# Kernel optimization log

Measured on AMD Instinct MI355X. Metric: run time of the kernel, lower is better.

Reference implementation:

```python
import jax, jax.numpy as jnp
from jax import lax
import numpy as np

B = 1024
CH = 32          # decomp.channel
LEVEL = 3        # decomp.level
CTOT = CH * (LEVEL + 1)   # 128, ODE state dim == GRU input dim
T_POINTS = 96    # decomp.eval_time_points
PRED_LEN = 96
HID = 128


def _dopri5_traj(y0, ts, Wo, bo):
    """Fixed-grid Dormand-Prince 5(4) integration of dy/dt = tanh(y Wo^T + bo).
    y0: [B, CTOT]; ts: [T]. Returns trajectory [T, B, CTOT]."""
    f = lambda y: jnp.tanh(y @ Wo.T + bo)

    def step(y, dt):
        k1 = f(y)
        k2 = f(y + dt * (0.2 * k1))
        k3 = f(y + dt * (3.0 / 40 * k1 + 9.0 / 40 * k2))
        k4 = f(y + dt * (44.0 / 45 * k1 - 56.0 / 15 * k2 + 32.0 / 9 * k3))
        k5 = f(y + dt * (19372.0 / 6561 * k1 - 25360.0 / 2187 * k2 + 64448.0 / 6561 * k3 - 212.0 / 729 * k4))
        k6 = f(y + dt * (9017.0 / 3168 * k1 - 355.0 / 33 * k2 + 46732.0 / 5247 * k3 + 49.0 / 176 * k4 - 5103.0 / 18656 * k5))
        y_next = y + dt * (35.0 / 384 * k1 + 500.0 / 1113 * k3 + 125.0 / 192 * k4 - 2187.0 / 6784 * k5 + 11.0 / 84 * k6)
        return y_next, y_next

    _, ys = lax.scan(step, y0, ts[1:] - ts[:-1])
    return jnp.concatenate([y0[None], ys], axis=0)


def _gru_layer(xs, W_ih, W_hh, b_ih, b_hh):
    """PyTorch-semantics GRU layer. xs: [T, B, D] -> hidden states [T, B, H]."""
    gi = jnp.einsum('tbd,gd->tbg', xs, W_ih) + b_ih  # precompute input gates
    H = W_hh.shape[1]

    def cell(h, gi_t):
        gh = h @ W_hh.T + b_hh
        i_r, i_z, i_n = jnp.split(gi_t, 3, axis=-1)
        h_r, h_z, h_n = jnp.split(gh, 3, axis=-1)
        r = jax.nn.sigmoid(i_r + h_r)
        z = jax.nn.sigmoid(i_z + h_z)
        n = jnp.tanh(i_n + r * h_n)
        h_new = (1.0 - z) * n + z * h
        return h_new, h_new

    h0 = jnp.zeros((xs.shape[1], H), xs.dtype)
    _, hs = lax.scan(cell, h0, gi)
    return hs


def setup_inputs() -> dict:
    key = jax.random.key(0)
    ks = jax.random.split(key, 20)
    s = 0.08  # ~1/sqrt(128), keeps GRU/ODE in a stable regime
    return {
        'x': jax.random.normal(ks[0], (B, CH, 256), jnp.float32),
        'yl': jax.random.normal(ks[1], (B, CH, 1), jnp.float32),
        'yh': jax.random.normal(ks[2], (B, CH * LEVEL, 1), jnp.float32),
        'W_ode': jax.random.normal(ks[3], (CTOT, CTOT), jnp.float32) * 0.05,
        'b_ode': jax.random.normal(ks[4], (CTOT,), jnp.float32) * 0.05,
        'W_ih0': jax.random.normal(ks[5], (3 * HID, CTOT), jnp.float32) * s,
        'W_hh0': jax.random.normal(ks[6], (3 * HID, HID), jnp.float32) * s,
        'b_ih0': jax.random.normal(ks[7], (3 * HID,), jnp.float32) * s,
        'b_hh0': jax.random.normal(ks[8], (3 * HID,), jnp.float32) * s,
        'W_ih1': jax.random.normal(ks[9], (3 * HID, HID), jnp.float32) * s,
        'W_hh1': jax.random.normal(ks[10], (3 * HID, HID), jnp.float32) * s,
        'b_ih1': jax.random.normal(ks[11], (3 * HID,), jnp.float32) * s,
        'b_hh1': jax.random.normal(ks[12], (3 * HID,), jnp.float32) * s,
        'W1': jax.random.normal(ks[13], (64, HID), jnp.float32) * s,
        'b1': jax.random.normal(ks[14], (64,), jnp.float32) * s,
        'W2': jax.random.normal(ks[15], (PRED_LEN * CH, 64), jnp.float32) * 0.125,
        'b2': jax.random.normal(ks[16], (PRED_LEN * CH,), jnp.float32) * 0.125,
    }


def reference(x, yl, yh, W_ode, b_ode,
              W_ih0, W_hh0, b_ih0, b_hh0,
              W_ih1, W_hh1, b_ih1, b_hh1,
              W1, b1, W2, b2):
    # coeffs = cat([yl] + yh, dim=1) -> [B, CTOT, 1] -> squeeze coeff length (=1)
    coeffs = jnp.concatenate([yl, yh], axis=1)[..., 0]  # [B, CTOT]
    ts = jnp.linspace(0.0, 1.0, T_POINTS)
    traj = _dopri5_traj(coeffs, ts, W_ode, b_ode)  # [T, B, CTOT]
    # rearrange 't b c l -> b t (c l)' with l == 1; GRU scans over leading T axis
    h1 = _gru_layer(traj, W_ih0, W_hh0, b_ih0, b_hh0)   # [T, B, HID]
    h2 = _gru_layer(h1, W_ih1, W_hh1, b_ih1, b_hh1)     # [T, B, HID]
    last = h2[-1]                                        # [B, HID]
    hidden = jax.nn.gelu(last @ W1.T + b1, approximate=False)
    pred = hidden @ W2.T + b2                            # [B, PRED_LEN*CH]
    return pred.reshape(-1, CH, PRED_LEN)
```

## Files before the change

kernel.cpp:

```cpp
#include <hip/hip_runtime.h>
#include <hip/hip_bf16.h>
#include <math.h>

#define TPTS 96
#define CTOT 128
#define LDP 134

typedef __bf16 bf16x8_t __attribute__((ext_vector_type(8)));
typedef float f32x4_t __attribute__((ext_vector_type(4)));
typedef unsigned short us8_t __attribute__((ext_vector_type(8)));

__device__ __forceinline__ unsigned short f2b(float f) {
    union { float f; unsigned int i; } v; v.f = f;
    unsigned int r = v.i + 0x7fffu + ((v.i >> 16) & 1u);
    return (unsigned short)(r >> 16);
}
__device__ __forceinline__ unsigned int packbf2(float a, float b) {
    return (unsigned int)f2b(a) | ((unsigned int)f2b(b) << 16);
}
__device__ __forceinline__ uint2 pack4(float v0, float v1, float v2, float v3) {
    uint2 w; w.x = packbf2(v0, v1); w.y = packbf2(v2, v3); return w;
}
__device__ __forceinline__ f32x4_t mfma16(bf16x8_t a, bf16x8_t b, f32x4_t c) {
    return __builtin_amdgcn_mfma_f32_16x16x32_bf16(a, b, c, 0, 0, 0);
}
__device__ __forceinline__ bf16x8_t ldfrag(const unsigned short* p) {
    us8_t v = *(const us8_t*)p;
    return __builtin_bit_cast(bf16x8_t, v);
}
__device__ __forceinline__ bf16x8_t ldfragG(const unsigned short* p) {
    union { unsigned long long q[2]; us8_t v; } u;
    u.q[0] = __hip_atomic_load((const unsigned long long*)p,
                               __ATOMIC_RELAXED, __HIP_MEMORY_SCOPE_AGENT);
    u.q[1] = __hip_atomic_load((const unsigned long long*)(p + 4),
                               __ATOMIC_RELAXED, __HIP_MEMORY_SCOPE_AGENT);
    return __builtin_bit_cast(bf16x8_t, u.v);
}
__device__ __forceinline__ void stg8(unsigned short* p, uint2 pk) {
    unsigned long long q = ((unsigned long long)pk.y << 32) | (unsigned long long)pk.x;
    __hip_atomic_store((unsigned long long*)p, q,
                       __ATOMIC_RELAXED, __HIP_MEMORY_SCOPE_AGENT);
}
__device__ __forceinline__ bf16x8_t ldfragW(const float* p) {
    float4 a = *(const float4*)p;
    float4 b = *(const float4*)(p + 4);
    bf16x8_t r;
    r[0] = __builtin_bit_cast(__bf16, f2b(a.x)); r[1] = __builtin_bit_cast(__bf16, f2b(a.y));
    r[2] = __builtin_bit_cast(__bf16, f2b(a.z)); r[3] = __builtin_bit_cast(__bf16, f2b(a.w));
    r[4] = __builtin_bit_cast(__bf16, f2b(b.x)); r[5] = __builtin_bit_cast(__bf16, f2b(b.y));
    r[6] = __builtin_bit_cast(__bf16, f2b(b.z)); r[7] = __builtin_bit_cast(__bf16, f2b(b.w));
    return r;
}
__device__ __forceinline__ float tanh2(float x) {
    float e = __expf(x + x);
    return 1.f - __fdividef(2.f, e + 1.f);
}
__device__ __forceinline__ float sigm(float x) {
    return __fdividef(1.f, 1.f + __expf(-x));
}

__device__ __forceinline__ void waitflag(unsigned int* f, unsigned int want) {
    if (threadIdx.x == 0) {
        int guard = 0;
        while (__hip_atomic_load(f, __ATOMIC_RELAXED, __HIP_MEMORY_SCOPE_AGENT) != want) {
            __builtin_amdgcn_s_sleep(2);
            if (++guard > (1 << 21)) break;
        }
    }
    __syncthreads();
}
__device__ __forceinline__ void setflag(unsigned int* f, unsigned int val) {
    if (threadIdx.x == 0) {
        asm volatile("s_waitcnt vmcnt(0)" ::: "memory");
        __hip_atomic_store(f, val, __ATOMIC_RELAXED, __HIP_MEMORY_SCOPE_AGENT);
    }
}

__global__ void __launch_bounds__(512, 2)
ode_forecaster(const float* __restrict__ yl,
               const float* __restrict__ yh,
               const float* __restrict__ Wode,
               const float* __restrict__ bode,
               const float* __restrict__ Wih0,
               const float* __restrict__ Whh0,
               const float* __restrict__ bih0,
               const float* __restrict__ bhh0,
               const float* __restrict__ Wih1,
               const float* __restrict__ Whh1,
               const float* __restrict__ bih1,
               const float* __restrict__ bhh1,
               const float* __restrict__ W1v,
               const float* __restrict__ b1v,
               const float* __restrict__ W2v,
               const float* __restrict__ b2v,
               float* __restrict__ outp,
               char* __restrict__ wsb)
{
    const int role = blockIdx.x >> 6;
    const int c    = blockIdx.x & 63;
    const int tid  = threadIdx.x, lane = tid & 63, wv = tid >> 6;
    const int l15  = lane & 15, quad = lane >> 4;
    const int fbase = wv * 16 + quad * 4;
    const int rbase = c * 16;

    __shared__ __align__(16) unsigned short zbuf[2][16][LDP];
    __shared__ __align__(16) unsigned short hidbuf[16][72];

    unsigned short* yTraj  = (unsigned short*)(wsb);
    unsigned short* h1Traj = (unsigned short*)(wsb + 0x2000000);
    unsigned int*   yflag  = (unsigned int*)(wsb + 0x4000000);
    unsigned int*   h1flag = (unsigned int*)(wsb + 0x4010000);
#define YMAGIC(t)  (0x5E000000u + (unsigned)(t))
#define H1MAGIC(t) (0x6E000000u + (unsigned)(t))

    if (role == 0) {
        bf16x8_t wode[4];
#pragma unroll
        for (int kt = 0; kt < 4; ++kt)
            wode[kt] = ldfragW(Wode + (wv * 16 + l15) * CTOT + kt * 32 + quad * 8);
        float bo[4];
        {
            float4 b4 = *(const float4*)(bode + fbase);
            bo[0] = b4.x; bo[1] = b4.y; bo[2] = b4.z; bo[3] = b4.w;
        }
        float y[4];
        {
            int row = rbase + l15;
#pragma unroll
            for (int i = 0; i < 4; ++i) {
                int f = fbase + i;
                y[i] = (f < 32) ? yl[row * 32 + f] : yh[row * 96 + (f - 32)];
            }
            uint2 pk = pack4(y[0], y[1], y[2], y[3]);
            *(uint2*)&zbuf[0][l15][fbase] = pk;
            stg8(yTraj + ((size_t)row) * CTOT + fbase, pk);
        }
        __syncthreads();
        setflag(&yflag[c * 128 + 0], YMAGIC(0));

        const float dt = 1.0f / 95.0f;
        const float d10 = dt * 0.2f;
        const float d20 = dt * (3.f/40.f),  d21 = dt * (9.f/40.f);
        const float d30 = dt * (44.f/45.f), d31 = dt * (-56.f/15.f), d32 = dt * (32.f/9.f);
        const float d40 = dt * (19372.f/6561.f), d41 = dt * (-25360.f/2187.f),
                    d42 = dt * (64448.f/6561.f), d43 = dt * (-212.f/729.f);
        const float d50 = dt * (9017.f/3168.f), d51 = dt * (-355.f/33.f),
                    d52 = dt * (46732.f/5247.f), d53 = dt * (49.f/176.f),
                    d54 = dt * (-5103.f/18656.f);
        const float e0 = dt * (35.f/384.f), e2 = dt * (500.f/1113.f), e3 = dt * (125.f/192.f),
                    e4 = dt * (-2187.f/6784.f), e5 = dt * (11.f/84.f);

        int p = 0;
        float kr[6][4];
#pragma unroll 1
        for (int t = 0; t < 95; ++t) {
#pragma unroll
            for (int s = 0; s < 6; ++s) {
                bf16x8_t bf[4];
#pragma unroll
                for (int kt = 0; kt < 4; ++kt)
                    bf[kt] = ldfrag(&zbuf[p][l15][kt * 32 + quad * 8]);
                f32x4_t a0 = {0.f, 0.f, 0.f, 0.f}, a1 = {0.f, 0.f, 0.f, 0.f};
                a0 = mfma16(wode[0], bf[0], a0);
                a1 = mfma16(wode[1], bf[1], a1);
                a0 = mfma16(wode[2], bf[2], a0);
                a1 = mfma16(wode[3], bf[3], a1);
                f32x4_t acc = a0 + a1;
#pragma unroll
                for (int i = 0; i < 4; ++i) kr[s][i] = tanh2(acc[i] + bo[i]);

                if (s < 5) {
                    float z[4];
#pragma unroll
                    for (int i = 0; i < 4; ++i) {
                        float zv;
                        if (s == 0)      zv = y[i] + d10 * kr[0][i];
                        else if (s == 1) zv = y[i] + d20 * kr[0][i] + d21 * kr[1][i];
                        else if (s == 2) zv = y[i] + d30 * kr[0][i] + d31 * kr[1][i] + d32 * kr[2][i];
                        else if (s == 3) zv = y[i] + d40 * kr[0][i] + d41 * kr[1][i]
                                             + d42 * kr[2][i] + d43 * kr[3][i];
                        else             zv = y[i] + d50 * kr[0][i] + d51 * kr[1][i]
                                             + d52 * kr[2][i] + d53 * kr[3][i] + d54 * kr[4][i];
                        z[i] = zv;
                    }
                    *(uint2*)&zbuf[p ^ 1][l15][fbase] = pack4(z[0], z[1], z[2], z[3]);
                } else {
#pragma unroll
                    for (int i = 0; i < 4; ++i)
                        y[i] += e0*kr[0][i] + e2*kr[2][i] + e3*kr[3][i] + e4*kr[4][i] + e5*kr[5][i];
                    uint2 pk = pack4(y[0], y[1], y[2], y[3]);
                    *(uint2*)&zbuf[p ^ 1][l15][fbase] = pk;
                    stg8(yTraj + ((size_t)(t + 1) * 1024 + rbase + l15) * CTOT + fbase, pk);
                }
                __syncthreads();
                p ^= 1;
                if (s == 5) setflag(&yflag[c * 128 + t + 1], YMAGIC(t + 1));
            }
        }
        return;
    }

    const float* Wih = (role == 1) ? Wih0 : Wih1;
    const float* Whh = (role == 1) ? Whh0 : Whh1;
    const float* bih = (role == 1) ? bih0 : bih1;
    const float* bhh = (role == 1) ? bhh0 : bhh1;
    const unsigned short* src = (role == 1) ? yTraj : h1Traj;
    unsigned int* sflag = (role == 1) ? yflag : h1flag;

    bf16x8_t wih[3][4], whh[3][4];
#pragma unroll
    for (int g = 0; g < 3; ++g)
#pragma unroll
        for (int kt = 0; kt < 4; ++kt) {
            wih[g][kt] = ldfragW(Wih + (size_t)(g * 128 + wv * 16 + l15) * CTOT + kt * 32 + quad * 8);
            whh[g][kt] = ldfragW(Whh + (size_t)(g * 128 + wv * 16 + l15) * CTOT + kt * 32 + quad * 8);
        }
    float br[4], bz[4], bin_[4], bhn[4];
    {
        float4 a0 = *(const float4*)(bih + 0 * 128 + fbase);
        float4 b0 = *(const float4*)(bhh + 0 * 128 + fbase);
        float4 a1 = *(const float4*)(bih + 1 * 128 + fbase);
        float4 b1 = *(const float4*)(bhh + 1 * 128 + fbase);
        float4 a2 = *(const float4*)(bih + 2 * 128 + fbase);
        float4 b2 = *(const float4*)(bhh + 2 * 128 + fbase);
        br[0] = a0.x + b0.x; br[1] = a0.y + b0.y; br[2] = a0.z + b0.z; br[3] = a0.w + b0.w;
        bz[0] = a1.x + b1.x; bz[1] = a1.y + b1.y; bz[2] = a1.z + b1.z; bz[3] = a1.w + b1.w;
        bin_[0] = a2.x; bin_[1] = a2.y; bin_[2] = a2.z; bin_[3] = a2.w;
        bhn[0] = b2.x; bhn[1] = b2.y; bhn[2] = b2.z; bhn[3] = b2.w;
    }

    float h[4] = {0.f, 0.f, 0.f, 0.f};
    *(uint2*)&zbuf[0][l15][fbase] = pack4(0.f, 0.f, 0.f, 0.f);
    int p = 0;
    __syncthreads();

#pragma unroll 1
    for (int t = 0; t < TPTS; ++t) {
        waitflag(&sflag[c * 128 + t], (role == 1) ? YMAGIC(t) : H1MAGIC(t));
        const unsigned short* xp = src + ((size_t)t * 1024 + rbase + l15) * CTOT;
        bf16x8_t ax[4], ah[4];
#pragma unroll
        for (int kt = 0; kt < 4; ++kt) {
            ax[kt] = ldfragG(xp + kt * 32 + quad * 8);
            ah[kt] = ldfrag(&zbuf[p][l15][kt * 32 + quad * 8]);
        }
        f32x4_t gx[3], gh[3];
#pragma unroll
        for (int g = 0; g < 3; ++g) {
            gx[g] = (f32x4_t){0.f, 0.f, 0.f, 0.f};
            gh[g] = (f32x4_t){0.f, 0.f, 0.f, 0.f};
        }
#pragma unroll
        for (int kt = 0; kt < 4; ++kt) {
            gx[0] = mfma16(wih[0][kt], ax[kt], gx[0]);
            gx[1] = mfma16(wih[1][kt], ax[kt], gx[1]);
            gx[2] = mfma16(wih[2][kt], ax[kt], gx[2]);
            gh[0] = mfma16(whh[0][kt], ah[kt], gh[0]);
            gh[1] = mfma16(whh[1][kt], ah[kt], gh[1]);
            gh[2] = mfma16(whh[2][kt], ah[kt], gh[2]);
        }
#pragma unroll
        for (int i = 0; i < 4; ++i) {
            float rr = sigm(gx[0][i] + gh[0][i] + br[i]);
            float zz = sigm(gx[1][i] + gh[1][i] + bz[i]);
            float nn = tanh2((gx[2][i] + bin_[i]) + rr * (gh[2][i] + bhn[i]));
            h[i] = nn + zz * (h[i] - nn);
        }
        uint2 pk = pack4(h[0], h[1], h[2], h[3]);
        *(uint2*)&zbuf[p ^ 1][l15][fbase] = pk;
        if (role == 1)
            stg8(h1Traj + ((size_t)t * 1024 + rbase + l15) * CTOT + fbase, pk);
        __syncthreads();
        if (role == 1) setflag(&h1flag[c * 128 + t], H1MAGIC(t));
        p ^= 1;
    }
    if (role == 1) return;

    if (wv < 4) {
        bf16x8_t wf[4], hf[4];
#pragma unroll
        for (int kt = 0; kt < 4; ++kt) {
            wf[kt] = ldfragW(W1v + (size_t)(wv * 16 + l15) * CTOT + kt * 32 + quad * 8);
            hf[kt] = ldfrag(&zbuf[p][l15][kt * 32 + quad * 8]);
        }
        f32x4_t acc = {0.f, 0.f, 0.f, 0.f};
#pragma unroll
        for (int kt = 0; kt < 4; ++kt) acc = mfma16(wf[kt], hf[kt], acc);
        float4 bb = *(const float4*)(b1v + wv * 16 + quad * 4);
        const float* bbp = (const float*)&bb;
        float gl[4];
#pragma unroll
        for (int i = 0; i < 4; ++i) {
            float x = acc[i] + bbp[i];
            gl[i] = 0.5f * x * (1.0f + erff(x * 0.70710678118654752f));
        }
        *(uint2*)&hidbuf[l15][wv * 16 + quad * 4] = pack4(gl[0], gl[1], gl[2], gl[3]);
    }
    __syncthreads();

    bf16x8_t ahid[2];
#pragma unroll
    for (int kt = 0; kt < 2; ++kt)
        ahid[kt] = ldfrag(&hidbuf[l15][kt * 32 + quad * 8]);
#pragma unroll 1
    for (int j = 0; j < 24; ++j) {
        int mt2 = wv * 24 + j;
        bf16x8_t wf0 = ldfragW(W2v + (size_t)(mt2 * 16 + l15) * 64 + quad * 8);
        bf16x8_t wf1 = ldfragW(W2v + (size_t)(mt2 * 16 + l15) * 64 + 32 + quad * 8);
        float4 bv = *(const float4*)(b2v + mt2 * 16 + quad * 4);
        const float* bvp = (const float*)&bv;
        f32x4_t acc = {0.f, 0.f, 0.f, 0.f};
        acc = mfma16(wf0, ahid[0], acc);
        acc = mfma16(wf1, ahid[1], acc);
        float4 o;
        o.x = acc[0] + bvp[0]; o.y = acc[1] + bvp[1];
        o.z = acc[2] + bvp[2]; o.w = acc[3] + bvp[3];
        *(float4*)(outp + (size_t)(rbase + l15) * 3072 + mt2 * 16 + quad * 4) = o;
    }
#undef YMAGIC
#undef H1MAGIC
}

extern "C" void kernel_launch(void* const* d_in, const int* in_sizes, int n_in,
                              void* d_out, int out_size, void* d_ws, size_t ws_size,
                              hipStream_t stream) {
    const float* yl   = (const float*)d_in[1];
    const float* yh   = (const float*)d_in[2];
    const float* Wode = (const float*)d_in[3];
    const float* bode = (const float*)d_in[4];
    const float* Wih0 = (const float*)d_in[5];
    const float* Whh0 = (const float*)d_in[6];
    const float* bih0 = (const float*)d_in[7];
    const float* bhh0 = (const float*)d_in[8];
    const float* Wih1 = (const float*)d_in[9];
    const float* Whh1 = (const float*)d_in[10];
    const float* bih1 = (const float*)d_in[11];
    const float* bhh1 = (const float*)d_in[12];
    const float* W1v  = (const float*)d_in[13];
    const float* b1v  = (const float*)d_in[14];
    const float* W2v  = (const float*)d_in[15];
    const float* b2v  = (const float*)d_in[16];

    ode_forecaster<<<dim3(192), dim3(512), 0, stream>>>(
        yl, yh, Wode, bode, Wih0, Whh0, bih0, bhh0,
        Wih1, Whh1, bih1, bhh1, W1v, b1v, W2v, b2v,
        (float*)d_out, (char*)d_ws);
}
```

Baseline: 768.4 us.

## Defer producer flag stores and use LDS-only barriers in ODE/GRU pipeline

Replaces __syncthreads plus an immediate vmcnt-draining flag store with lgkmcnt-only barriers. The vmcnt wait and the flag publish are deferred to a later substep or timestep, so global-store latency overlaps with compute. The bf16 pack now uses the hardware v_cvt_pk_bf16_f32 instruction, the ODE MFMA chain is split into four independent accumulators, and the tanh bias is folded into an fma. The GRU layer 1 loop is split out as its own specialized loop. Consumers now see readiness slightly later, and correctness relies on ordering the waitcnt before the flag store.

```diff
diff --git a/kernel.cpp b/kernel.cpp
--- a/kernel.cpp
+++ b/kernel.cpp
@@ -16,7 +16,9 @@
     return (unsigned short)(r >> 16);
 }
 __device__ __forceinline__ unsigned int packbf2(float a, float b) {
-    return (unsigned int)f2b(a) | ((unsigned int)f2b(b) << 16);
+    unsigned int r;
+    asm("v_cvt_pk_bf16_f32 %0, %1, %2" : "=v"(r) : "v"(a), "v"(b));
+    return r;
 }
 __device__ __forceinline__ uint2 pack4(float v0, float v1, float v2, float v3) {
     uint2 w; w.x = packbf2(v0, v1); w.y = packbf2(v2, v3); return w;
@@ -59,12 +61,17 @@
     return __fdividef(1.f, 1.f + __expf(-x));
 }
 
+#define LGKM_BAR() do {                                         \
+        asm volatile("s_waitcnt lgkmcnt(0)" ::: "memory");      \
+        __builtin_amdgcn_s_barrier();                           \
+    } while (0)
+
 __device__ __forceinline__ void waitflag(unsigned int* f, unsigned int want) {
     if (threadIdx.x == 0) {
         int guard = 0;
         while (__hip_atomic_load(f, __ATOMIC_RELAXED, __HIP_MEMORY_SCOPE_AGENT) != want) {
-            __builtin_amdgcn_s_sleep(2);
-            if (++guard > (1 << 21)) break;
+            __builtin_amdgcn_s_sleep(1);
+            if (++guard > (1 << 22)) break;
         }
     }
     __syncthreads();
@@ -118,10 +125,10 @@
 #pragma unroll
         for (int kt = 0; kt < 4; ++kt)
             wode[kt] = ldfragW(Wode + (wv * 16 + l15) * CTOT + kt * 32 + quad * 8);
-        float bo[4];
+        float bo2[4];
         {
             float4 b4 = *(const float4*)(bode + fbase);
-            bo[0] = b4.x; bo[1] = b4.y; bo[2] = b4.z; bo[3] = b4.w;
+            bo2[0] = 2.f * b4.x; bo2[1] = 2.f * b4.y; bo2[2] = 2.f * b4.z; bo2[3] = 2.f * b4.w;
         }
         float y[4];
         {
@@ -160,14 +167,17 @@
 #pragma unroll
                 for (int kt = 0; kt < 4; ++kt)
                     bf[kt] = ldfrag(&zbuf[p][l15][kt * 32 + quad * 8]);
-                f32x4_t a0 = {0.f, 0.f, 0.f, 0.f}, a1 = {0.f, 0.f, 0.f, 0.f};
-                a0 = mfma16(wode[0], bf[0], a0);
-                a1 = mfma16(wode[1], bf[1], a1);
-                a0 = mfma16(wode[2], bf[2], a0);
-                a1 = mfma16(wode[3], bf[3], a1);
-                f32x4_t acc = a0 + a1;
-#pragma unroll
-                for (int i = 0; i < 4; ++i) kr[s][i] = tanh2(acc[i] + bo[i]);
+                const f32x4_t zz = {0.f, 0.f, 0.f, 0.f};
+                f32x4_t a0 = mfma16(wode[0], bf[0], zz);
+                f32x4_t a1 = mfma16(wode[1], bf[1], zz);
+                f32x4_t a2 = mfma16(wode[2], bf[2], zz);
+                f32x4_t a3 = mfma16(wode[3], bf[3], zz);
+                f32x4_t acc = (a0 + a1) + (a2 + a3);
+#pragma unroll
+                for (int i = 0; i < 4; ++i) {
+                    float e = __expf(fmaf(acc[i], 2.f, bo2[i]));
+                    kr[s][i] = 1.f - __fdividef(2.f, e + 1.f);
+                }
 
                 if (s < 5) {
                     float z[4];
@@ -192,11 +202,20 @@
                     *(uint2*)&zbuf[p ^ 1][l15][fbase] = pk;
                     stg8(yTraj + ((size_t)(t + 1) * 1024 + rbase + l15) * CTOT + fbase, pk);
                 }
-                __syncthreads();
+                if (s == 1)
+                    asm volatile("s_waitcnt vmcnt(0)" ::: "memory");
+                LGKM_BAR();
+                if (s == 1 && t > 0 && tid == 0)
+                    __hip_atomic_store(&yflag[c * 128 + t], YMAGIC(t),
+                                       __ATOMIC_RELAXED, __HIP_MEMORY_SCOPE_AGENT);
                 p ^= 1;
-                if (s == 5) setflag(&yflag[c * 128 + t + 1], YMAGIC(t + 1));
-            }
-        }
+            }
+        }
+        asm volatile("s_waitcnt vmcnt(0)" ::: "memory");
+        __builtin_amdgcn_s_barrier();
+        if (tid == 0)
+            __hip_atomic_store(&yflag[c * 128 + 95], YMAGIC(95),
+                               __ATOMIC_RELAXED, __HIP_MEMORY_SCOPE_AGENT);
         return;
     }
 
@@ -234,9 +253,69 @@
     int p = 0;
     __syncthreads();
 
+    if (role == 1) {
+#pragma unroll 1
+        for (int t = 0; t < TPTS; ++t) {
+            asm volatile("s_waitcnt vmcnt(0)" ::: "memory");
+            __builtin_amdgcn_s_barrier();
+            if (tid == 0) {
+                if (t > 0)
+                    __hip_atomic_store(&h1flag[c * 128 + (t - 1)], H1MAGIC(t - 1),
+                                       __ATOMIC_RELAXED, __HIP_MEMORY_SCOPE_AGENT);
+                int guard = 0;
+                while (__hip_atomic_load(&yflag[c * 128 + t],
+                                         __ATOMIC_RELAXED, __HIP_MEMORY_SCOPE_AGENT) != YMAGIC(t)) {
+                    __builtin_amdgcn_s_sleep(1);
+                    if (++guard > (1 << 22)) break;
+                }
+            }
+            __syncthreads();
+            const unsigned short* xp = src + ((size_t)t * 1024 + rbase + l15) * CTOT;
+            bf16x8_t ax[4], ah[4];
+#pragma unroll
+            for (int kt = 0; kt < 4; ++kt) {
+                ax[kt] = ldfragG(xp + kt * 32 + quad * 8);
+                ah[kt] = ldfrag(&zbuf[p][l15][kt * 32 + quad * 8]);
+            }
+            f32x4_t gx[3], gh[3];
+#pragma unroll
+            for (int g = 0; g < 3; ++g) {
+                gx[g] = (f32x4_t){0.f, 0.f, 0.f, 0.f};
+                gh[g] = (f32x4_t){0.f, 0.f, 0.f, 0.f};
+            }
+#pragma unroll
+            for (int kt = 0; kt < 4; ++kt) {
+                gx[0] = mfma16(wih[0][kt], ax[kt], gx[0]);
+                gx[1] = mfma16(wih[1][kt], ax[kt], gx[1]);
+                gx[2] = mfma16(wih[2][kt], ax[kt], gx[2]);
+                gh[0] = mfma16(whh[0][kt], ah[kt], gh[0]);
+                gh[1] = mfma16(whh[1][kt], ah[kt], gh[1]);
+                gh[2] = mfma16(whh[2][kt], ah[kt], gh[2]);
+            }
+#pragma unroll
+            for (int i = 0; i < 4; ++i) {
+                float rr = sigm(gx[0][i] + gh[0][i] + br[i]);
+                float zz = sigm(gx[1][i] + gh[1][i] + bz[i]);
+                float nn = tanh2((gx[2][i] + bin_[i]) + rr * (gh[2][i] + bhn[i]));
+                h[i] = nn + zz * (h[i] - nn);
+            }
+            uint2 pk = pack4(h[0], h[1], h[2], h[3]);
+            *(uint2*)&zbuf[p ^ 1][l15][fbase] = pk;
+            stg8(h1Traj + ((size_t)t * 1024 + rbase + l15) * CTOT + fbase, pk);
+            LGKM_BAR();
+            p ^= 1;
+        }
+        asm volatile("s_waitcnt vmcnt(0)" ::: "memory");
+        __syncthreads();
+        if (tid == 0)
+            __hip_atomic_store(&h1flag[c * 128 + (TPTS - 1)], H1MAGIC(TPTS - 1),
+                               __ATOMIC_RELAXED, __HIP_MEMORY_SCOPE_AGENT);
+        return;
+    }
+
 #pragma unroll 1
     for (int t = 0; t < TPTS; ++t) {
-        waitflag(&sflag[c * 128 + t], (role == 1) ? YMAGIC(t) : H1MAGIC(t));
+        waitflag(&sflag[c * 128 + t], H1MAGIC(t));
         const unsigned short* xp = src + ((size_t)t * 1024 + rbase + l15) * CTOT;
         bf16x8_t ax[4], ah[4];
 #pragma unroll
@@ -266,15 +345,10 @@
             float nn = tanh2((gx[2][i] + bin_[i]) + rr * (gh[2][i] + bhn[i]));
             h[i] = nn + zz * (h[i] - nn);
         }
-        uint2 pk = pack4(h[0], h[1], h[2], h[3]);
-        *(uint2*)&zbuf[p ^ 1][l15][fbase] = pk;
-        if (role == 1)
-            stg8(h1Traj + ((size_t)t * 1024 + rbase + l15) * CTOT + fbase, pk);
-        __syncthreads();
-        if (role == 1) setflag(&h1flag[c * 128 + t], H1MAGIC(t));
+        *(uint2*)&zbuf[p ^ 1][l15][fbase] = pack4(h[0], h[1], h[2], h[3]);
+        LGKM_BAR();
         p ^= 1;
     }
-    if (role == 1) return;
 
     if (wv < 4) {
         bf16x8_t wf[4], hf[4];
```

After: 764.3 us (median of 2 runs). No clear change (-0.5%).
